# Kernel optimization log

Hardware: AMD Instinct MI355X
Metric: run time of the kernel (lower is better)

## Reference

```python
import jax, jax.numpy as jnp
import numpy as np

DIM = 1024
HEADS = 16
BLK = 129
DK = 64
DV = 64
B = 4
N = BLK * 32  # 4128


def setup_inputs() -> dict:
    key = jax.random.key(0)
    ks = jax.random.split(key, 6)
    inner_k = HEADS * DK
    inner_v = HEADS * DV
    s = 1.0 / np.sqrt(DIM)
    x = jax.random.normal(ks[0], (B, N, DIM), dtype=jnp.float32)
    Wq = jax.random.normal(ks[1], (inner_k, DIM), dtype=jnp.float32) * s
    Wk = jax.random.normal(ks[2], (inner_k, DIM), dtype=jnp.float32) * s
    Wv = jax.random.normal(ks[3], (inner_v, DIM), dtype=jnp.float32) * s
    Wo = jax.random.normal(ks[4], (DIM, inner_v), dtype=jnp.float32) * (1.0 / np.sqrt(inner_v))
    bo = jax.random.normal(ks[5], (DIM,), dtype=jnp.float32) * 0.01
    return {"x": x, "Wq": Wq, "Wk": Wk, "Wv": Wv, "Wo": Wo, "bo": bo}


def reference(x, Wq, Wk, Wv, Wo, bo):
    Bsz, Nlen, D = x.shape
    nb = Nlen // BLK
    scale = 1.0 / np.sqrt(DK)
    # projections (Linear without bias: x @ W.T)
    q = (x @ Wq.T).reshape(Bsz, nb, BLK, HEADS, DK)
    k = (x @ Wk.T).reshape(Bsz, nb, BLK, HEADS, DK)
    v = (x @ Wv.T).reshape(Bsz, nb, BLK, HEADS, DV)
    # block-local attention: each block attends within itself
    scores = jnp.einsum('bnqhd,bnkhd->bnhqk', q, k) * scale  # [B,nb,H,BLK,BLK]
    attn = jax.nn.softmax(scores, axis=-1)
    out_blk = jnp.einsum('bnhqk,bnkhd->bnhqd', attn, v)  # [B,nb,H,BLK,DV]
    # global attention among the first token of each block
    qg = q[:, :, 0]  # [B,nb,H,DK]
    kg = k[:, :, 0]
    vg = v[:, :, 0]
    sg = jnp.einsum('bqhd,bkhd->bhqk', qg, kg) * scale  # [B,H,nb,nb]
    ag = jax.nn.softmax(sg, axis=-1)
    out_g = jnp.einsum('bhqk,bkhd->bqhd', ag, vg)  # [B,nb,H,DV]
    # add global output onto position 0 of each block
    out_blk = out_blk.at[:, :, :, 0, :].add(out_g.transpose(0, 1, 2, 3).swapaxes(2, 2))  # out_g already [B,nb,H,DV]
    # reassemble to [B,N,H*DV]
    out = out_blk.transpose(0, 1, 3, 2, 4).reshape(Bsz, Nlen, HEADS * DV)
    return out @ Wo.T + bo
```

## Files before the change

kernel.cpp:

```cpp
#include <hip/hip_runtime.h>

typedef unsigned short u16;
typedef __attribute__((ext_vector_type(8))) __bf16 bf16x8;
typedef __attribute__((ext_vector_type(4))) float f32x4;
typedef __attribute__((ext_vector_type(8))) u16 u16x8;
typedef __attribute__((ext_vector_type(4))) u16 u16x4;

#define DIMSZ 1024
#define HEADS 16
#define BLKSZ 129
#define NBLK 32
#define NTOK (BLKSZ * NBLK)
#define BATCH 4
#define MROWS (BATCH * NTOK)

#define MFMA __builtin_amdgcn_mfma_f32_16x16x32_bf16

#define SSTR 152
#define KSTR 72

#define NKT 32

__device__ __forceinline__ float bf2f(u16 u) {
  return __uint_as_float(((unsigned)u) << 16);
}
__device__ __forceinline__ u16 f2bf(float f) {
  unsigned u = __float_as_uint(f);
  u += 0x7FFFu + ((u >> 16) & 1u);
  return (u16)(u >> 16);
}

#define GLD16(ldsp, gp) __builtin_amdgcn_global_load_lds( \
    (const __attribute__((address_space(1))) void*)(gp),   \
    (__attribute__((address_space(3))) void*)(ldsp), 16, 0, 0)

__global__ __launch_bounds__(256) void cast_f32_bf16(
    const float* __restrict__ in, u16* __restrict__ out, int n)
{
  int i = (blockIdx.x * 256 + threadIdx.x) * 4;
  if (i < n) {
    float4 f = *(const float4*)(in + i);
    u16x4 o = { f2bf(f.x), f2bf(f.y), f2bf(f.z), f2bf(f.w) };
    *(u16x4*)(out + i) = o;
  }
}

__device__ __forceinline__ int xcd_swz(int bid, int nwg) {
  const int xcd = bid & 7, l = bid >> 3;
  const int q = nwg >> 3, r = nwg & 7;
  return (xcd < r ? xcd * (q + 1) : r * (q + 1) + (xcd - r) * q) + l;
}

__device__ __forceinline__ void stage_slot(u16* slot, const u16* gA,
                                           const u16* gB, int tid) {
  GLD16(slot + tid * 8, gA);
  GLD16(slot + 4096 + tid * 8, gA + 128 * DIMSZ);
  GLD16(slot + 8192 + tid * 8, gB);
  GLD16(slot + 12288 + tid * 8, gB + 128 * DIMSZ);
}

__device__ __forceinline__ void gemm_pipe256(
    const u16* __restrict__ A, const u16* __restrict__ Bm,
    int m0, int n0, int tid, u16 (*sm)[16384], f32x4 (*acc)[4])
{
  const int lane = tid & 63, w = tid >> 6;
  const int qd = lane >> 4, l15 = lane & 15;
  const int wm = (w >> 2) * 128, wn = (w & 3) * 64;
  const int qdsw = (qd ^ ((l15 >> 1) & 3)) * 8;

  const int srow = tid >> 2;
  const int schk = (tid & 3) ^ ((tid >> 3) & 3);
  const u16* gA = A + (size_t)(m0 + srow) * DIMSZ + schk * 8;
  const u16* gB = Bm + (size_t)(n0 + srow) * DIMSZ + schk * 8;

  stage_slot(sm[0], gA, gB, tid);
  stage_slot(sm[1], gA + 32, gB + 32, tid);
  asm volatile("s_waitcnt vmcnt(4)" ::: "memory");
  __builtin_amdgcn_s_barrier();
  __builtin_amdgcn_sched_barrier(0);

#pragma unroll 4
  for (int t = 0; t < NKT; ++t) {
    if (t + 2 < NKT)
      stage_slot(sm[(t + 2) & 3], gA + (t + 2) * 32, gB + (t + 2) * 32, tid);

    const u16* sA = sm[t & 3];
    const u16* sB = sm[t & 3] + 8192;
    bf16x8 af[8], bv[4];
#pragma unroll
    for (int mi = 0; mi < 8; ++mi)
      af[mi] = *(const bf16x8*)&sA[(wm + mi * 16 + l15) * 32 + qdsw];
#pragma unroll
    for (int ni = 0; ni < 4; ++ni)
      bv[ni] = *(const bf16x8*)&sB[(wn + ni * 16 + l15) * 32 + qdsw];

    __builtin_amdgcn_s_setprio(1);
#pragma unroll
    for (int mi = 0; mi < 8; ++mi)
#pragma unroll
      for (int ni = 0; ni < 4; ++ni)
        acc[mi][ni] = MFMA(af[mi], bv[ni], acc[mi][ni], 0, 0, 0);
    __builtin_amdgcn_s_setprio(0);

    __builtin_amdgcn_sched_barrier(0);
    if (t + 2 < NKT) {
      asm volatile("s_waitcnt vmcnt(4)" ::: "memory");
    } else {
      asm volatile("s_waitcnt vmcnt(0)" ::: "memory");
    }
    __builtin_amdgcn_s_barrier();
    __builtin_amdgcn_sched_barrier(0);
  }
}

__global__ __launch_bounds__(512, 2) void gemm_qkv(
    const u16* __restrict__ A, const u16* __restrict__ B,
    u16* __restrict__ Cq, u16* __restrict__ Ck, u16* __restrict__ Cv)
{
  __shared__ u16 sm[4][16384];
  const int tid = threadIdx.x;
  f32x4 acc[8][4];
#pragma unroll
  for (int mi = 0; mi < 8; ++mi)
#pragma unroll
    for (int ni = 0; ni < 4; ++ni)
      acc[mi][ni] = (f32x4){0.f, 0.f, 0.f, 0.f};

  const int wg = xcd_swz(blockIdx.x, 65 * 12);
  const int nt = wg % 12, mt = wg / 12;
  const int m0 = mt * 256, n0 = nt * 256;

  gemm_pipe256(A, B, m0, n0, tid, sm, acc);

  u16* C = nt < 4 ? Cq : (nt < 8 ? Ck : Cv);
  const int c0 = (nt & 3) * 256;
  const int lane = tid & 63, w = tid >> 6;
  const int qd = lane >> 4, l15 = lane & 15;
  const int wm = (w >> 2) * 128, wn = (w & 3) * 64;
#pragma unroll
  for (int mi = 0; mi < 8; ++mi)
#pragma unroll
    for (int ni = 0; ni < 4; ++ni) {
      const int row0 = m0 + wm + mi * 16 + qd * 4;
      const int col  = c0 + wn + ni * 16 + l15;
#pragma unroll
      for (int r = 0; r < 4; ++r)
        if (row0 + r < MROWS)
          C[(size_t)(row0 + r) * DIMSZ + col] = f2bf(acc[mi][ni][r]);
    }
}

__global__ __launch_bounds__(512, 2) void gemm_out(
    const u16* __restrict__ A, const u16* __restrict__ B,
    float* __restrict__ C, const float* __restrict__ bias)
{
  __shared__ u16 sm[4][16384];
  const int tid = threadIdx.x;
  f32x4 acc[8][4];
#pragma unroll
  for (int mi = 0; mi < 8; ++mi)
#pragma unroll
    for (int ni = 0; ni < 4; ++ni)
      acc[mi][ni] = (f32x4){0.f, 0.f, 0.f, 0.f};

  const int wg = xcd_swz(blockIdx.x, 65 * 4);
  const int nt = wg % 4, mt = wg / 4;
  const int m0 = mt * 256, n0 = nt * 256;

  gemm_pipe256(A, B, m0, n0, tid, sm, acc);

  const int lane = tid & 63, w = tid >> 6;
  const int qd = lane >> 4, l15 = lane & 15;
  const int wm = (w >> 2) * 128, wn = (w & 3) * 64;
#pragma unroll
  for (int mi = 0; mi < 8; ++mi)
#pragma unroll
    for (int ni = 0; ni < 4; ++ni) {
      const int row0 = m0 + wm + mi * 16 + qd * 4;
      const int col  = n0 + wn + ni * 16 + l15;
      float badd = bias[col];
#pragma unroll
      for (int r = 0; r < 4; ++r)
        if (row0 + r < MROWS)
          C[(size_t)(row0 + r) * DIMSZ + col] = acc[mi][ni][r] + badd;
    }
}

__global__ __launch_bounds__(64) void global_attn(
    const u16* __restrict__ q, const u16* __restrict__ k,
    const u16* __restrict__ v, float* __restrict__ g)
{
  __shared__ float sQ[NBLK * 64];
  __shared__ float sKT[64 * NBLK];
  __shared__ float sV[NBLK * 64];
  __shared__ float sp[NBLK];
  const int b = blockIdx.x >> 4, h = blockIdx.x & 15;
  const int lane = threadIdx.x;

  for (int idx = lane; idx < NBLK * 64; idx += 64) {
    int j = idx >> 6, d = idx & 63;
    size_t off = ((size_t)(b * NTOK + j * BLKSZ)) * DIMSZ + h * 64 + d;
    sQ[idx] = bf2f(q[off]);
    sKT[d * NBLK + j] = bf2f(k[off]);
    sV[idx] = bf2f(v[off]);
  }
  __syncthreads();

  for (int i = 0; i < NBLK; ++i) {
    float s = -3.0e38f;
    if (lane < 32) {
      float acc = 0.f;
      for (int d = 0; d < 64; ++d) acc += sQ[i * 64 + d] * sKT[d * NBLK + lane];
      s = acc * 0.125f;
    }
    float m = s;
    for (int t = 1; t < 64; t <<= 1) m = fmaxf(m, __shfl_xor(m, t));
    float e = (lane < 32) ? __expf(s - m) : 0.f;
    float sum = e;
    for (int t = 1; t < 64; t <<= 1) sum += __shfl_xor(sum, t);
    if (lane < 32) sp[lane] = e / sum;
    __syncthreads();
    float acc = 0.f;
    for (int jj = 0; jj < NBLK; ++jj) acc += sp[jj] * sV[jj * 64 + lane];
    g[(((size_t)b * NBLK + i) * HEADS + h) * 64 + lane] = acc;
    __syncthreads();
  }
}

__global__ __launch_bounds__(512) void block_attn(
    const u16* q, const u16* __restrict__ k,
    const u16* __restrict__ v, const float* __restrict__ g,
    u16* ao)
{
  __shared__ u16 sS[144 * SSTR];
  __shared__ u16 sKV[144 * KSTR];
  const int b = blockIdx.x, blk = blockIdx.y, h = blockIdx.z;
  const int tid = threadIdx.x, lane = tid & 63, w = tid >> 6;
  const int qd = lane >> 4, l15 = lane & 15;
  const int h64 = h * 64;
  const size_t row_base = (size_t)b * NTOK + (size_t)blk * BLKSZ;
  const f32x4 zero4 = {0.f, 0.f, 0.f, 0.f};

  {
    const u16x8 zero8 = {0, 0, 0, 0, 0, 0, 0, 0};
    for (int c = tid; c < 144 * 8; c += 512) {
      int row = c >> 3, cc = c & 7;
      u16x8 val = zero8;
      if (row < BLKSZ)
        val = *(const u16x8*)(k + (row_base + row) * DIMSZ + h64 + cc * 8);
      *(u16x8*)&sKV[row * KSTR + cc * 8] = val;
    }
  }
  __syncthreads();

  for (int t = w; t < 81; t += 8) {
    int mt = t / 9, nt = t - mt * 9;
    int qrow = mt * 16 + l15;
    if (qrow > 128) qrow = 128;
    const u16* qp = q + (row_base + qrow) * DIMSZ + h64;
    bf16x8 qf0 = *(const bf16x8*)(qp + qd * 8);
    bf16x8 qf1 = *(const bf16x8*)(qp + 32 + qd * 8);
    bf16x8 kf0 = *(const bf16x8*)&sKV[(nt * 16 + l15) * KSTR + qd * 8];
    bf16x8 kf1 = *(const bf16x8*)&sKV[(nt * 16 + l15) * KSTR + 32 + qd * 8];
    f32x4 c = zero4;
    c = MFMA(qf0, kf0, c, 0, 0, 0);
    c = MFMA(qf1, kf1, c, 0, 0, 0);
    int r0 = mt * 16 + qd * 4, col = nt * 16 + l15;
#pragma unroll
    for (int r = 0; r < 4; ++r)
      sS[(r0 + r) * SSTR + col] = f2bf(c[r] * 0.125f);
  }
  __syncthreads();

  for (int c = tid; c < BLKSZ * 8; c += 512) {
    int row = c >> 3, cc = c & 7;
    u16x8 val = *(const u16x8*)(v + (row_base + row) * DIMSZ + h64 + cc * 8);
#pragma unroll
    for (int jj = 0; jj < 8; ++jj)
      sKV[(cc * 8 + jj) * SSTR + row] = val[jj];
  }

  for (int row = w; row < BLKSZ; row += 8) {
    float x1 = bf2f(sS[row * SSTR + lane]);
    float x2 = bf2f(sS[row * SSTR + 64 + lane]);
    float x3 = (lane == 0) ? bf2f(sS[row * SSTR + 128]) : -3.0e38f;
    float m = fmaxf(fmaxf(x1, x2), x3);
    for (int t = 1; t < 64; t <<= 1) m = fmaxf(m, __shfl_xor(m, t));
    float e1 = __expf(x1 - m), e2 = __expf(x2 - m);
    float e3 = (lane == 0) ? __expf(x3 - m) : 0.f;
    float s = e1 + e2 + e3;
    for (int t = 1; t < 64; t <<= 1) s += __shfl_xor(s, t);
    float inv = 1.f / s;
    sS[row * SSTR + lane] = f2bf(e1 * inv);
    sS[row * SSTR + 64 + lane] = f2bf(e2 * inv);
    if (lane == 0) sS[row * SSTR + 128] = f2bf(e3 * inv);
  }
  __syncthreads();

  for (int t = w; t < 36; t += 8) {
    int mt = t >> 2, nt = t & 3;
    f32x4 c = zero4;
#pragma unroll
    for (int kk = 0; kk < 128; kk += 32) {
      bf16x8 pf = *(const bf16x8*)&sS[(mt * 16 + l15) * SSTR + kk + qd * 8];
      bf16x8 vf = *(const bf16x8*)&sKV[(nt * 16 + l15) * SSTR + kk + qd * 8];
      c = MFMA(pf, vf, c, 0, 0, 0);
    }
    int dv = nt * 16 + l15;
    float v128 = bf2f(sKV[dv * SSTR + 128]);
    int r0 = mt * 16 + qd * 4;
#pragma unroll
    for (int r = 0; r < 4; ++r) {
      int row = r0 + r;
      if (row < BLKSZ) {
        float p128 = bf2f(sS[row * SSTR + 128]);
        float val = c[r] + p128 * v128;
        if (row == 0)
          val += g[(((size_t)b * NBLK + blk) * HEADS + h) * 64 + dv];
        ao[(row_base + row) * DIMSZ + h64 + dv] = f2bf(val);
      }
    }
  }
}

extern "C" void kernel_launch(void* const* d_in, const int* in_sizes, int n_in,
                              void* d_out, int out_size, void* d_ws, size_t ws_size,
                              hipStream_t stream) {
  const float* x  = (const float*)d_in[0];
  const float* Wq = (const float*)d_in[1];
  const float* Wk = (const float*)d_in[2];
  const float* Wv = (const float*)d_in[3];
  const float* Wo = (const float*)d_in[4];
  const float* bo = (const float*)d_in[5];
  float* out = (float*)d_out;

  char* ws = (char*)d_ws;
  const size_t xb = (size_t)MROWS * DIMSZ * sizeof(u16);
  float* gb     = (float*)ws;
  u16*   qb     = (u16*)(ws + (1u << 20));
  u16*   x16    = (u16*)(ws + (1u << 20) + xb);
  u16*   Wqkv16 = (u16*)(ws + (1u << 20) + 2 * xb);
  u16*   Wo16   = x16;
  u16*   kb     = (u16*)d_out;
  u16*   vb     = (u16*)d_out + (size_t)MROWS * DIMSZ;

  const int nx = MROWS * DIMSZ;
  const int nw = DIMSZ * DIMSZ;
  cast_f32_bf16<<<nx / 1024, 256, 0, stream>>>(x,  x16, nx);
  cast_f32_bf16<<<nw / 1024, 256, 0, stream>>>(Wq, Wqkv16,          nw);
  cast_f32_bf16<<<nw / 1024, 256, 0, stream>>>(Wk, Wqkv16 + nw,     nw);
  cast_f32_bf16<<<nw / 1024, 256, 0, stream>>>(Wv, Wqkv16 + 2 * nw, nw);

  gemm_qkv<<<dim3(65 * 12), 512, 0, stream>>>(x16, Wqkv16, qb, kb, vb);

  cast_f32_bf16<<<nw / 1024, 256, 0, stream>>>(Wo, Wo16, nw);

  global_attn<<<dim3(BATCH * HEADS), 64, 0, stream>>>(qb, kb, vb, gb);
  block_attn<<<dim3(BATCH, NBLK, HEADS), 512, 0, stream>>>(qb, kb, vb, gb, qb);
  gemm_out<<<dim3(65 * 4), 512, 0, stream>>>(qb, Wo16, out, bo);
}
```

Baseline: 484.8 us.

## Split 256-tile GEMM loop into two interleaved halves; use 128-row tiles for output GEMM

The main 256x256 GEMM pipeline now splits each k-step into two halves. Each half issues part of the next-slot global loads, then runs its MFMA group, with extra barriers in between, so memory traffic is spread across compute. The output projection GEMM moves to a new 128x256-tile, triple-buffered pipeline with more workgroups (129*4 instead of 65*4) and a higher occupancy hint. The goal is better load/compute overlap and fuller use of the compute units. In exchange it adds more barriers per iteration, and the row bounds check in the output store is removed; 129*128 rows equals MROWS exactly, so this is still in bounds.

```diff
diff --git a/kernel.cpp b/kernel.cpp
--- a/kernel.cpp
+++ b/kernel.cpp
@@ -81,35 +81,124 @@
 
 #pragma unroll 4
   for (int t = 0; t < NKT; ++t) {
-    if (t + 2 < NKT)
-      stage_slot(sm[(t + 2) & 3], gA + (t + 2) * 32, gB + (t + 2) * 32, tid);
-
     const u16* sA = sm[t & 3];
     const u16* sB = sm[t & 3] + 8192;
-    bf16x8 af[8], bv[4];
-#pragma unroll
-    for (int mi = 0; mi < 8; ++mi)
+    u16* sl2 = sm[(t + 2) & 3];
+    const u16* gA2 = gA + (t + 2) * 32;
+    const u16* gB2 = gB + (t + 2) * 32;
+    const bool pf = (t + 2 < NKT);
+
+    bf16x8 af[4], bv[4];
+#pragma unroll
+    for (int mi = 0; mi < 4; ++mi)
       af[mi] = *(const bf16x8*)&sA[(wm + mi * 16 + l15) * 32 + qdsw];
 #pragma unroll
     for (int ni = 0; ni < 4; ++ni)
       bv[ni] = *(const bf16x8*)&sB[(wn + ni * 16 + l15) * 32 + qdsw];
-
+    if (pf) {
+      GLD16(sl2 + tid * 8, gA2);
+      GLD16(sl2 + 4096 + tid * 8, gA2 + 128 * DIMSZ);
+    }
+    __builtin_amdgcn_sched_barrier(0);
+    __builtin_amdgcn_s_barrier();
     __builtin_amdgcn_s_setprio(1);
 #pragma unroll
-    for (int mi = 0; mi < 8; ++mi)
+    for (int mi = 0; mi < 4; ++mi)
 #pragma unroll
       for (int ni = 0; ni < 4; ++ni)
         acc[mi][ni] = MFMA(af[mi], bv[ni], acc[mi][ni], 0, 0, 0);
     __builtin_amdgcn_s_setprio(0);
-
-    __builtin_amdgcn_sched_barrier(0);
-    if (t + 2 < NKT) {
+    __builtin_amdgcn_sched_barrier(0);
+
+    bf16x8 ag[4];
+#pragma unroll
+    for (int mi = 0; mi < 4; ++mi)
+      ag[mi] = *(const bf16x8*)&sA[(wm + 64 + mi * 16 + l15) * 32 + qdsw];
+    if (pf) {
+      GLD16(sl2 + 8192 + tid * 8, gB2);
+      GLD16(sl2 + 12288 + tid * 8, gB2 + 128 * DIMSZ);
+    }
+    __builtin_amdgcn_sched_barrier(0);
+    __builtin_amdgcn_s_barrier();
+    __builtin_amdgcn_s_setprio(1);
+#pragma unroll
+    for (int mi = 0; mi < 4; ++mi)
+#pragma unroll
+      for (int ni = 0; ni < 4; ++ni)
+        acc[mi + 4][ni] = MFMA(ag[mi], bv[ni], acc[mi + 4][ni], 0, 0, 0);
+    __builtin_amdgcn_s_setprio(0);
+    __builtin_amdgcn_sched_barrier(0);
+
+    if (pf) {
       asm volatile("s_waitcnt vmcnt(4)" ::: "memory");
     } else {
       asm volatile("s_waitcnt vmcnt(0)" ::: "memory");
     }
     __builtin_amdgcn_s_barrier();
     __builtin_amdgcn_sched_barrier(0);
+  }
+}
+
+__device__ __forceinline__ void stage_slot128(u16* slot, const u16* gA,
+                                              const u16* gB, int tid) {
+  GLD16(slot + tid * 8, gA);
+  GLD16(slot + 4096 + tid * 8, gB);
+  GLD16(slot + 8192 + tid * 8, gB + 128 * DIMSZ);
+}
+
+__device__ __forceinline__ void gemm_pipe128(
+    const u16* __restrict__ A, const u16* __restrict__ Bm,
+    int m0, int n0, int tid, u16 (*sm)[12288], f32x4 (*acc)[4])
+{
+  const int lane = tid & 63, w = tid >> 6;
+  const int qd = lane >> 4, l15 = lane & 15;
+  const int wm = (w >> 2) * 64, wn = (w & 3) * 64;
+  const int qdsw = (qd ^ ((l15 >> 1) & 3)) * 8;
+
+  const int srow = tid >> 2;
+  const int schk = (tid & 3) ^ ((tid >> 3) & 3);
+  const u16* gA = A + (size_t)(m0 + srow) * DIMSZ + schk * 8;
+  const u16* gB = Bm + (size_t)(n0 + srow) * DIMSZ + schk * 8;
+
+  u16 *p0 = sm[0], *p1 = sm[1], *p2 = sm[2];
+  stage_slot128(p0, gA, gB, tid);
+  stage_slot128(p1, gA + 32, gB + 32, tid);
+  asm volatile("s_waitcnt vmcnt(3)" ::: "memory");
+  __builtin_amdgcn_s_barrier();
+  __builtin_amdgcn_sched_barrier(0);
+
+  for (int t = 0; t < NKT; ++t) {
+    const bool pf = (t + 2 < NKT);
+    if (pf)
+      stage_slot128(p2, gA + (t + 2) * 32, gB + (t + 2) * 32, tid);
+
+    bf16x8 af[4], bv[4];
+#pragma unroll
+    for (int mi = 0; mi < 4; ++mi)
+      af[mi] = *(const bf16x8*)&p0[(wm + mi * 16 + l15) * 32 + qdsw];
+#pragma unroll
+    for (int ni = 0; ni < 4; ++ni)
+      bv[ni] = *(const bf16x8*)&p0[4096 + (wn + ni * 16 + l15) * 32 + qdsw];
+
+    __builtin_amdgcn_sched_barrier(0);
+    __builtin_amdgcn_s_setprio(1);
+#pragma unroll
+    for (int mi = 0; mi < 4; ++mi)
+#pragma unroll
+      for (int ni = 0; ni < 4; ++ni)
+        acc[mi][ni] = MFMA(af[mi], bv[ni], acc[mi][ni], 0, 0, 0);
+    __builtin_amdgcn_s_setprio(0);
+    __builtin_amdgcn_sched_barrier(0);
+
+    if (pf) {
+      asm volatile("s_waitcnt vmcnt(3)" ::: "memory");
+    } else {
+      asm volatile("s_waitcnt vmcnt(0)" ::: "memory");
+    }
+    __builtin_amdgcn_s_barrier();
+    __builtin_amdgcn_sched_barrier(0);
+
+    u16* tmp = p0; p0 = p1; p1 = p2; p2 = tmp;
   }
 }
 
@@ -150,30 +239,30 @@
     }
 }
 
-__global__ __launch_bounds__(512, 2) void gemm_out(
+__global__ __launch_bounds__(512, 4) void gemm_out(
     const u16* __restrict__ A, const u16* __restrict__ B,
     float* __restrict__ C, const float* __restrict__ bias)
 {
-  __shared__ u16 sm[4][16384];
+  __shared__ u16 sm[3][12288];
   const int tid = threadIdx.x;
-  f32x4 acc[8][4];
-#pragma unroll
-  for (int mi = 0; mi < 8; ++mi)
+  f32x4 acc[4][4];
+#pragma unroll
+  for (int mi = 0; mi < 4; ++mi)
 #pragma unroll
     for (int ni = 0; ni < 4; ++ni)
       acc[mi][ni] = (f32x4){0.f, 0.f, 0.f, 0.f};
 
-  const int wg = xcd_swz(blockIdx.x, 65 * 4);
-  const int nt = wg % 4, mt = wg / 4;
-  const int m0 = mt * 256, n0 = nt * 256;
-
-  gemm_pipe256(A, B, m0, n0, tid, sm, acc);
+  const int wg = xcd_swz(blockIdx.x, 129 * 4);
+  const int nt = wg & 3, mt = wg >> 2;
+  const int m0 = mt * 128, n0 = nt * 256;
+
+  gemm_pipe128(A, B, m0, n0, tid, sm, acc);
 
   const int lane = tid & 63, w = tid >> 6;
   const int qd = lane >> 4, l15 = lane & 15;
-  const int wm = (w >> 2) * 128, wn = (w & 3) * 64;
-#pragma unroll
-  for (int mi = 0; mi < 8; ++mi)
+  const int wm = (w >> 2) * 64, wn = (w & 3) * 64;
+#pragma unroll
+  for (int mi = 0; mi < 4; ++mi)
 #pragma unroll
     for (int ni = 0; ni < 4; ++ni) {
       const int row0 = m0 + wm + mi * 16 + qd * 4;
@@ -181,8 +270,7 @@
       float badd = bias[col];
 #pragma unroll
       for (int r = 0; r < 4; ++r)
-        if (row0 + r < MROWS)
-          C[(size_t)(row0 + r) * DIMSZ + col] = acc[mi][ni][r] + badd;
+        C[(size_t)(row0 + r) * DIMSZ + col] = acc[mi][ni][r] + badd;
     }
 }
 
@@ -357,5 +445,5 @@
 
   global_attn<<<dim3(BATCH * HEADS), 64, 0, stream>>>(qb, kb, vb, gb);
   block_attn<<<dim3(BATCH, NBLK, HEADS), 512, 0, stream>>>(qb, kb, vb, gb, qb);
-  gemm_out<<<dim3(65 * 4), 512, 0, stream>>>(qb, Wo16, out, bo);
-}
+  gemm_out<<<dim3(129 * 4), 512, 0, stream>>>(qb, Wo16, out, bo);
+}
```

Measured after the change: 466.7 us. -3.7%, faster.
